# Performance work log

Hardware: AMD Instinct MI355X
Metric: run time of the kernel (lower is better)

The kernel has to match this reference:

```python
import jax, jax.numpy as jnp
import numpy as np

N_HEAD = 16

def setup_inputs() -> dict:
    key = jax.random.key(0)
    k1, k2, k3, k4, k5 = jax.random.split(key, 5)
    B, T, C = 8, 2048, 1024
    hs = C // N_HEAD  # 64
    return {
        "ids": jax.random.normal(k1, (B, T, C), dtype=jnp.float32),
        "qkv_w": jax.random.normal(k2, (3 * hs, C), dtype=jnp.float32) * (C ** -0.5),
        "qkv_b": jax.random.normal(k3, (3 * hs,), dtype=jnp.float32) * 0.02,
        "proj_w": jax.random.normal(k4, (C, C), dtype=jnp.float32) * (C ** -0.5),
        "proj_b": jax.random.normal(k5, (C,), dtype=jnp.float32) * 0.02,
    }

def reference(ids, qkv_w, qkv_b, proj_w, proj_b):
    B, T, C = ids.shape
    hs = qkv_w.shape[0] // 3  # head_size
    # All heads share the same qkv Linear (input is replicated per-head in the
    # original), so compute one head and tile at the end.
    qkv = ids @ qkv_w.T + qkv_b                      # [B,T,3*hs]
    q, k, v = jnp.split(qkv, 3, axis=-1)             # each [B,T,hs]
    wei = jnp.einsum('btd,bsd->bts', q, k)           # [B,T,T]
    tril = jnp.tril(jnp.ones((T, T), dtype=bool))
    wei = jnp.where(tril, wei, jnp.float32(0.0))     # causal mask (no softmax)
    out_h = jnp.einsum('bts,bsd->btd', wei, v)       # [B,T,hs]
    out = jnp.tile(out_h, (1, 1, N_HEAD))            # identical heads concatenated
    return out @ proj_w.T + proj_b                   # [B,T,C]
```

## Files before the change

### kernel.cpp

```cpp
#include <hip/hip_runtime.h>
#include <hip/hip_bf16.h>

#define Bsz 8
#define Tsz 2048
#define Csz 1024
#define HSsz 64
#define NQ 192

typedef __attribute__((ext_vector_type(8))) short short8v;
typedef __attribute__((ext_vector_type(4))) float f32x4;
typedef unsigned short ushortT;
typedef unsigned int uintT;

__device__ __forceinline__ unsigned int f2bf(float f) {
    union { float f; unsigned int u; } v; v.f = f;
    return (v.u + 0x7fffu + ((v.u >> 16) & 1u)) >> 16;
}

__device__ __forceinline__ unsigned int pk2bf(float lo, float hi) {
    union { __hip_bfloat162 h2; unsigned int u; } cv;
    cv.h2 = __float22bfloat162_rn(float2{lo, hi});
    return cv.u;
}

__global__ __launch_bounds__(256) void k_prep(const float* __restrict__ qw,
                                              const float* __restrict__ pw,
                                              ushortT* __restrict__ wB,
                                              ushortT* __restrict__ w2a) {
    const int blk = blockIdx.x;
    if (blk < 96) {
        int idx = blk * 256 + threadIdx.x;
        int l = idx & 63;
        int ksjt = idx >> 6;
        int jt = ksjt % 12, ks = ksjt / 12;
        int j = jt * 16 + (l & 15);
        int k = ks * 32 + (l >> 4) * 8;
        const float* src = &qw[j * Csz + k];
        float4 a = *(const float4*)src;
        float4 b = *(const float4*)(src + 4);
        uint4 o;
        o.x = f2bf(a.x) | (f2bf(a.y) << 16);
        o.y = f2bf(a.z) | (f2bf(a.w) << 16);
        o.z = f2bf(b.x) | (f2bf(b.y) << 16);
        o.w = f2bf(b.z) | (f2bf(b.w) << 16);
        *(uint4*)&wB[(size_t)idx * 8] = o;
    } else {
        int idx = (blk - 96) * 256 + threadIdx.x;
        int l = idx & 63;
        int rest = idx >> 6;
        int m = rest & 63, ks = rest >> 6;
        int c = m * 16 + (l & 15);
        int d0 = ks * 32 + (l >> 4) * 8;
        float s0 = 0, s1 = 0, s2 = 0, s3 = 0, s4 = 0, s5 = 0, s6 = 0, s7 = 0;
#pragma unroll
        for (int hh = 0; hh < 16; ++hh) {
            const float* p = &pw[c * Csz + hh * HSsz + d0];
            float4 x = *(const float4*)p;
            float4 y = *(const float4*)(p + 4);
            s0 += x.x; s1 += x.y; s2 += x.z; s3 += x.w;
            s4 += y.x; s5 += y.y; s6 += y.z; s7 += y.w;
        }
        uint4 o;
        o.x = f2bf(s0) | (f2bf(s1) << 16);
        o.y = f2bf(s2) | (f2bf(s3) << 16);
        o.z = f2bf(s4) | (f2bf(s5) << 16);
        o.w = f2bf(s6) | (f2bf(s7) << 16);
        *(uint4*)&w2a[(size_t)idx * 8] = o;
    }
}

__global__ __launch_bounds__(512, 4) void k_qkv_mfma(const float* __restrict__ ids,
                                                     const ushortT* __restrict__ wB,
                                                     const float* __restrict__ bias,
                                                     ushortT* __restrict__ Qf,
                                                     ushortT* __restrict__ Kf,
                                                     ushortT* __restrict__ Vf) {
    __shared__ float sA[2][32 * 132];
    uintT* Lqk = (uintT*)&sA[0][0];
    uintT* Lv  = Lqk + 32 * 68;

    const int tid = threadIdx.x;
    const int wv  = tid >> 6;
    const int l   = tid & 63;
    const int wm  = wv >> 2;
    const int wn  = wv & 3;
    const int lg  = l >> 4, ll = l & 15;

    const int row0 = blockIdx.x * 32;

    const int srow = tid >> 4;
    const int scol = (tid & 15) * 8;
    const float* gsrc = ids + (size_t)(row0 + srow) * Csz + scol;

    const int afrow = wm * 16 + ll;

    f32x4 acc[3];
    acc[0] = acc[1] = acc[2] = (f32x4){0.f, 0.f, 0.f, 0.f};

    float4 st0 = *(const float4*)gsrc;
    float4 st1 = *(const float4*)(gsrc + 4);

    const ushortT* bbase_p = wB + ((size_t)(wn * 3) * 64 + l) * 8;

    for (int c = 0; c < 8; ++c) {
        float* bufp = &sA[c & 1][0];
        float* wp = &bufp[srow * 132 + scol];
        *(float4*)wp = st0;
        *(float4*)(wp + 4) = st1;
        __syncthreads();
        if (c < 7) {
            st0 = *(const float4*)(gsrc + (c + 1) * 128);
            st1 = *(const float4*)(gsrc + (c + 1) * 128 + 4);
        }
#pragma unroll
        for (int kk = 0; kk < 4; ++kk) {
            const ushortT* bp = bbase_p + (size_t)(4 * c + kk) * 6144;
            short8v b0 = *(const short8v*)(bp);
            short8v b1 = *(const short8v*)(bp + 512);
            short8v b2 = *(const short8v*)(bp + 1024);

            const float* ap = &bufp[afrow * 132 + kk * 32 + lg * 8];
            float4 a0 = *(const float4*)ap;
            float4 a1 = *(const float4*)(ap + 4);
            union { short8v s; unsigned int u[4]; } af;
            af.u[0] = pk2bf(a0.x, a0.y); af.u[1] = pk2bf(a0.z, a0.w);
            af.u[2] = pk2bf(a1.x, a1.y); af.u[3] = pk2bf(a1.z, a1.w);

            acc[0] = __builtin_amdgcn_mfma_f32_16x16x32_bf16(af.s, b0, acc[0], 0, 0, 0);
            acc[1] = __builtin_amdgcn_mfma_f32_16x16x32_bf16(af.s, b1, acc[1], 0, 0, 0);
            acc[2] = __builtin_amdgcn_mfma_f32_16x16x32_bf16(af.s, b2, acc[2], 0, 0, 0);
        }
    }
    __syncthreads();

    const int crow_l = wm * 16 + lg * 4;
    ushortT* L16 = (ushortT*)Lqk;
#pragma unroll
    for (int n = 0; n < 3; ++n) {
        const int jb = wn * 3 + n;
        const int j  = jb * 16 + ll;
        const float bj = bias[j];
        float v0 = acc[n][0] + bj, v1 = acc[n][1] + bj;
        float v2 = acc[n][2] + bj, v3 = acc[n][3] + bj;
        if (jb < 8) {
            ushortT* p = &L16[crow_l * 136 + j];
            p[0]   = (ushortT)f2bf(v0);
            p[136] = (ushortT)f2bf(v1);
            p[272] = (ushortT)f2bf(v2);
            p[408] = (ushortT)f2bf(v3);
        } else {
            uintT* p = &Lv[(j - 128) * 20 + (crow_l >> 1)];
            p[0] = pk2bf(v0, v1);
            p[1] = pk2bf(v2, v3);
        }
    }
    __syncthreads();

    const int l2 = tid & 63, ll2 = l2 & 15, lg2 = l2 >> 4;
    if (tid < 256) {
        const int ks = (tid >> 6) & 1, m = tid >> 7;
        uint4 q = *(const uint4*)&Lqk[(m * 16 + ll2) * 68 + ks * 16 + lg2 * 4];
        *(uint4*)&Qf[(((size_t)(row0 >> 4) + m) * 2 + ks) * 512 + l2 * 8] = q;
        const int n = tid >> 6;
        uint4 v = *(const uint4*)&Lv[(n * 16 + ll2) * 20 + lg2 * 4];
        const int bb = row0 >> 11, s32 = (row0 >> 5) & 63;
        *(uint4*)&Vf[((((size_t)bb * 64 + s32) * 4 + n) * 64 + l2) * 8] = v;
    } else {
        const int ks = (tid >> 6) & 1, m = (tid >> 7) & 1;
        uint4 k = *(const uint4*)&Lqk[(m * 16 + ll2) * 68 + 32 + ks * 16 + lg2 * 4];
        *(uint4*)&Kf[(((size_t)(row0 >> 4) + m) * 2 + ks) * 512 + l2 * 8] = k;
    }
}

__global__ __launch_bounds__(256, 3) void k_attn_mfma(const ushortT* __restrict__ Qf,
                                                      const ushortT* __restrict__ Kf,
                                                      const ushortT* __restrict__ Vf,
                                                      ushortT* __restrict__ hf) {
    __shared__ uintT su[4 * 2 * 16 * 36];
    __shared__ float s_o[4][32 * 68];

    const int tid = threadIdx.x;
    const int w  = tid >> 6;
    const int l  = tid & 63;
    const int lg = l >> 4;
    const int ll = l & 15;

    const int u = blockIdx.x;
    const int b = u / 48;
    const int r = u - b * 48;

    int si, sub, nsub;
    const bool heavy = (r < 32);
    if (heavy) { si = 63 - r; sub = w; nsub = 4; }
    else {
        const int rr = r - 32;
        si = (w < 2) ? (31 - rr) : rr;
        sub = w & 1; nsub = 2;
    }
    const int nT  = (si >> 1) + 1;
    const int qn  = nT / nsub, rem = nT % nsub;
    const int t0  = sub * qn + (sub < rem ? sub : rem);
    const int cnt = qn + (sub < rem ? 1 : 0);

    const int gq = b * 128 + si * 2;

    short8v qf[2][2];
#pragma unroll
    for (int mt = 0; mt < 2; ++mt)
#pragma unroll
        for (int ks = 0; ks < 2; ++ks)
            qf[mt][ks] = *(const short8v*)&Qf[(((size_t)gq + mt) * 2 + ks) * 512 + l * 8];

    f32x4 oacc[2][4];
#pragma unroll
    for (int mt = 0; mt < 2; ++mt)
#pragma unroll
        for (int n = 0; n < 4; ++n) oacc[mt][n] = (f32x4){0.f, 0.f, 0.f, 0.f};

    for (int tile = t0; tile < t0 + cnt; ++tile) {
        const int gs = b * 128 + tile * 4;
        short8v kf[4][2];
#pragma unroll
        for (int ms = 0; ms < 4; ++ms) {
            const ushortT* kp = &Kf[(((size_t)gs + ms) * 2) * 512 + l * 8];
            kf[ms][0] = *(const short8v*)kp;
            kf[ms][1] = *(const short8v*)(kp + 512);
        }
        f32x4 sacc[4][2];
#pragma unroll
        for (int ms = 0; ms < 4; ++ms)
#pragma unroll
            for (int mt = 0; mt < 2; ++mt) sacc[ms][mt] = (f32x4){0.f, 0.f, 0.f, 0.f};
#pragma unroll
        for (int ms = 0; ms < 4; ++ms)
#pragma unroll
            for (int mt = 0; mt < 2; ++mt) {
                sacc[ms][mt] = __builtin_amdgcn_mfma_f32_16x16x32_bf16(kf[ms][0], qf[mt][0], sacc[ms][mt], 0, 0, 0);
                sacc[ms][mt] = __builtin_amdgcn_mfma_f32_16x16x32_bf16(kf[ms][1], qf[mt][1], sacc[ms][mt], 0, 0, 0);
            }
        if (tile == nT - 1) {
#pragma unroll
            for (int ms = 0; ms < 4; ++ms)
#pragma unroll
                for (int mt = 0; mt < 2; ++mt) {
                    const int tg = si * 32 + mt * 16 + ll;
#pragma unroll
                    for (int rr2 = 0; rr2 < 4; ++rr2) {
                        int sg = tile * 64 + ms * 16 + 4 * lg + rr2;
                        if (sg > tg) sacc[ms][mt][rr2] = 0.f;
                    }
                }
        }
#pragma unroll
        for (int mt = 0; mt < 2; ++mt)
#pragma unroll
            for (int ms = 0; ms < 4; ++ms) {
                uint2 pk;
                pk.x = pk2bf(sacc[ms][mt][0], sacc[ms][mt][1]);
                pk.y = pk2bf(sacc[ms][mt][2], sacc[ms][mt][3]);
                *(uint2*)&su[((w * 2 + mt) * 16 + ll) * 36 + ms * 8 + 2 * lg] = pk;
            }
        union { uint4 u4; short8v s; } pa[2][2];
#pragma unroll
        for (int mt = 0; mt < 2; ++mt)
#pragma unroll
            for (int h = 0; h < 2; ++h)
                pa[mt][h].u4 = *(const uint4*)&su[((w * 2 + mt) * 16 + ll) * 36 + h * 16 + lg * 4];

        const int gv = b * 64 + tile * 2;
        short8v vf[2][4];
#pragma unroll
        for (int h = 0; h < 2; ++h)
#pragma unroll
            for (int n = 0; n < 4; ++n)
                vf[h][n] = *(const short8v*)&Vf[((((size_t)gv + h) * 4 + n) * 64 + l) * 8];
#pragma unroll
        for (int mt = 0; mt < 2; ++mt)
#pragma unroll
            for (int n = 0; n < 4; ++n) {
                oacc[mt][n] = __builtin_amdgcn_mfma_f32_16x16x32_bf16(pa[mt][0].s, vf[0][n], oacc[mt][n], 0, 0, 0);
                oacc[mt][n] = __builtin_amdgcn_mfma_f32_16x16x32_bf16(pa[mt][1].s, vf[1][n], oacc[mt][n], 0, 0, 0);
            }
    }

#pragma unroll
    for (int mt = 0; mt < 2; ++mt)
#pragma unroll
        for (int n = 0; n < 4; ++n)
#pragma unroll
            for (int rr2 = 0; rr2 < 4; ++rr2)
                s_o[w][(mt * 16 + 4 * lg + rr2) * 68 + 16 * n + ll] = oacc[mt][n][rr2];
    __syncthreads();

    const int l2 = tid & 63, ll2 = l2 & 15, lg2 = l2 >> 4;
    const int ks = (tid >> 6) & 1, mt = tid >> 7;
    const int t = mt * 16 + ll2, dd = ks * 32 + lg2 * 8;
    if (heavy) {
        float4 A = {0, 0, 0, 0}, B2 = {0, 0, 0, 0};
#pragma unroll
        for (int w2 = 0; w2 < 4; ++w2) {
            const float4 x = *(const float4*)&s_o[w2][t * 68 + dd];
            const float4 y = *(const float4*)&s_o[w2][t * 68 + dd + 4];
            A.x += x.x; A.y += x.y; A.z += x.z; A.w += x.w;
            B2.x += y.x; B2.y += y.y; B2.z += y.z; B2.w += y.w;
        }
        uint4 o;
        o.x = pk2bf(A.x, A.y);  o.y = pk2bf(A.z, A.w);
        o.z = pk2bf(B2.x, B2.y); o.w = pk2bf(B2.z, B2.w);
        *(uint4*)&hf[(((size_t)(b * 128 + si * 2) + mt) * 2 + ks) * 512 + l2 * 8] = o;
    } else {
        const int rr = r - 32;
        const int sa = 31 - rr, sb = rr;
        float4 A = {0, 0, 0, 0}, B2 = {0, 0, 0, 0};
#pragma unroll
        for (int w2 = 0; w2 < 2; ++w2) {
            const float4 x = *(const float4*)&s_o[w2][t * 68 + dd];
            const float4 y = *(const float4*)&s_o[w2][t * 68 + dd + 4];
            A.x += x.x; A.y += x.y; A.z += x.z; A.w += x.w;
            B2.x += y.x; B2.y += y.y; B2.z += y.z; B2.w += y.w;
        }
        uint4 o;
        o.x = pk2bf(A.x, A.y);  o.y = pk2bf(A.z, A.w);
        o.z = pk2bf(B2.x, B2.y); o.w = pk2bf(B2.z, B2.w);
        *(uint4*)&hf[(((size_t)(b * 128 + sa * 2) + mt) * 2 + ks) * 512 + l2 * 8] = o;
        float4 C = {0, 0, 0, 0}, D2 = {0, 0, 0, 0};
#pragma unroll
        for (int w2 = 2; w2 < 4; ++w2) {
            const float4 x = *(const float4*)&s_o[w2][t * 68 + dd];
            const float4 y = *(const float4*)&s_o[w2][t * 68 + dd + 4];
            C.x += x.x; C.y += x.y; C.z += x.z; C.w += x.w;
            D2.x += y.x; D2.y += y.y; D2.z += y.z; D2.w += y.w;
        }
        uint4 o2;
        o2.x = pk2bf(C.x, C.y);  o2.y = pk2bf(C.z, C.w);
        o2.z = pk2bf(D2.x, D2.y); o2.w = pk2bf(D2.z, D2.w);
        *(uint4*)&hf[(((size_t)(b * 128 + sb * 2) + mt) * 2 + ks) * 512 + l2 * 8] = o2;
    }
}

__global__ __launch_bounds__(256) void k_proj_mfma(const ushortT* __restrict__ hf,
                                                   const ushortT* __restrict__ w2a,
                                                   const float* __restrict__ pb,
                                                   float* __restrict__ out) {
    const int tid = threadIdx.x;
    const int w = tid >> 6, l = tid & 63;
    const int t0 = blockIdx.x * 16;
    const size_t M = blockIdx.x;

    short8v hb0 = *(const short8v*)&hf[(M * 2 + 0) * 512 + l * 8];
    short8v hb1 = *(const short8v*)&hf[(M * 2 + 1) * 512 + l * 8];

    const int row = (l >> 4) * 4;
    const int tcol = l & 15;
    const size_t outrow = (size_t)(t0 + tcol) * Csz;

#pragma unroll 2
    for (int m = w * 16; m < w * 16 + 16; ++m) {
        const ushortT* ap = w2a + (size_t)(m * 64 + l) * 8;
        short8v a0 = *(const short8v*)ap;
        short8v a1 = *(const short8v*)(ap + 32768);
        f32x4 acc = (f32x4){0.f, 0.f, 0.f, 0.f};
        acc = __builtin_amdgcn_mfma_f32_16x16x32_bf16(a0, hb0, acc, 0, 0, 0);
        acc = __builtin_amdgcn_mfma_f32_16x16x32_bf16(a1, hb1, acc, 0, 0, 0);
        const int c0 = m * 16 + row;
        const float4 pv = *(const float4*)&pb[c0];
        float4 o;
        o.x = acc[0] + pv.x; o.y = acc[1] + pv.y;
        o.z = acc[2] + pv.z; o.w = acc[3] + pv.w;
        *(float4*)&out[outrow + c0] = o;
    }
}

extern "C" void kernel_launch(void* const* d_in, const int* in_sizes, int n_in,
                              void* d_out, int out_size, void* d_ws, size_t ws_size,
                              hipStream_t stream) {
    const float* ids    = (const float*)d_in[0];
    const float* qkv_w  = (const float*)d_in[1];
    const float* qkv_b  = (const float*)d_in[2];
    const float* proj_w = (const float*)d_in[3];
    const float* proj_b = (const float*)d_in[4];
    float* out = (float*)d_out;

    ushortT* Qf  = (ushortT*)d_ws;
    ushortT* Kf  = Qf + 16384 * HSsz;
    ushortT* Vf  = Kf + 16384 * HSsz;
    ushortT* hf  = Vf + 16384 * HSsz;
    ushortT* wB  = hf + 16384 * HSsz;
    ushortT* w2a = wB + 196608;

    hipLaunchKernelGGL(k_prep,      dim3(128),  dim3(256), 0, stream, qkv_w, proj_w, wB, w2a);
    hipLaunchKernelGGL(k_qkv_mfma,  dim3(512),  dim3(512), 0, stream, ids, wB, qkv_b, Qf, Kf, Vf);
    hipLaunchKernelGGL(k_attn_mfma, dim3(384),  dim3(256), 0, stream, Qf, Kf, Vf, hf);
    hipLaunchKernelGGL(k_proj_mfma, dim3(1024), dim3(256), 0, stream, hf, w2a, proj_b, out);
}
```

Baseline: 63.44 us.

## Simplify attention block scheduling and process two row tiles per projection block

Attention now launches one block per 32-row query tile, ordered heaviest-first, with the four waves splitting key tiles. This replaces the heavy/light pairing scheme and removes its branchy reduction code. The projection kernel handles two 16-row tiles per block so each loaded weight fragment feeds two MFMA chains, halving weight reads and block count. Light attention blocks may leave waves underused, and the projection keeps more accumulators live.

Measured after the change: 60.16 us, median of 2. -5.2%, faster.

```diff
diff --git a/kernel.cpp b/kernel.cpp
--- a/kernel.cpp
+++ b/kernel.cpp
@@ -186,21 +186,13 @@
     const int ll = l & 15;
 
     const int u = blockIdx.x;
-    const int b = u / 48;
-    const int r = u - b * 48;
-
-    int si, sub, nsub;
-    const bool heavy = (r < 32);
-    if (heavy) { si = 63 - r; sub = w; nsub = 4; }
-    else {
-        const int rr = r - 32;
-        si = (w < 2) ? (31 - rr) : rr;
-        sub = w & 1; nsub = 2;
-    }
+    const int b = u & 7;
+    const int si = 63 - (u >> 3);
+
     const int nT  = (si >> 1) + 1;
-    const int qn  = nT / nsub, rem = nT % nsub;
-    const int t0  = sub * qn + (sub < rem ? sub : rem);
-    const int cnt = qn + (sub < rem ? 1 : 0);
+    const int qn  = nT >> 2, rem = nT & 3;
+    const int t0  = w * qn + (w < rem ? w : rem);
+    const int cnt = qn + (w < rem ? 1 : 0);
 
     const int gq = b * 128 + si * 2;
 
@@ -295,47 +287,18 @@
     const int l2 = tid & 63, ll2 = l2 & 15, lg2 = l2 >> 4;
     const int ks = (tid >> 6) & 1, mt = tid >> 7;
     const int t = mt * 16 + ll2, dd = ks * 32 + lg2 * 8;
-    if (heavy) {
-        float4 A = {0, 0, 0, 0}, B2 = {0, 0, 0, 0};
-#pragma unroll
-        for (int w2 = 0; w2 < 4; ++w2) {
-            const float4 x = *(const float4*)&s_o[w2][t * 68 + dd];
-            const float4 y = *(const float4*)&s_o[w2][t * 68 + dd + 4];
-            A.x += x.x; A.y += x.y; A.z += x.z; A.w += x.w;
-            B2.x += y.x; B2.y += y.y; B2.z += y.z; B2.w += y.w;
-        }
-        uint4 o;
-        o.x = pk2bf(A.x, A.y);  o.y = pk2bf(A.z, A.w);
-        o.z = pk2bf(B2.x, B2.y); o.w = pk2bf(B2.z, B2.w);
-        *(uint4*)&hf[(((size_t)(b * 128 + si * 2) + mt) * 2 + ks) * 512 + l2 * 8] = o;
-    } else {
-        const int rr = r - 32;
-        const int sa = 31 - rr, sb = rr;
-        float4 A = {0, 0, 0, 0}, B2 = {0, 0, 0, 0};
-#pragma unroll
-        for (int w2 = 0; w2 < 2; ++w2) {
-            const float4 x = *(const float4*)&s_o[w2][t * 68 + dd];
-            const float4 y = *(const float4*)&s_o[w2][t * 68 + dd + 4];
-            A.x += x.x; A.y += x.y; A.z += x.z; A.w += x.w;
-            B2.x += y.x; B2.y += y.y; B2.z += y.z; B2.w += y.w;
-        }
-        uint4 o;
-        o.x = pk2bf(A.x, A.y);  o.y = pk2bf(A.z, A.w);
-        o.z = pk2bf(B2.x, B2.y); o.w = pk2bf(B2.z, B2.w);
-        *(uint4*)&hf[(((size_t)(b * 128 + sa * 2) + mt) * 2 + ks) * 512 + l2 * 8] = o;
-        float4 C = {0, 0, 0, 0}, D2 = {0, 0, 0, 0};
-#pragma unroll
-        for (int w2 = 2; w2 < 4; ++w2) {
-            const float4 x = *(const float4*)&s_o[w2][t * 68 + dd];
-            const float4 y = *(const float4*)&s_o[w2][t * 68 + dd + 4];
-            C.x += x.x; C.y += x.y; C.z += x.z; C.w += x.w;
-            D2.x += y.x; D2.y += y.y; D2.z += y.z; D2.w += y.w;
-        }
-        uint4 o2;
-        o2.x = pk2bf(C.x, C.y);  o2.y = pk2bf(C.z, C.w);
-        o2.z = pk2bf(D2.x, D2.y); o2.w = pk2bf(D2.z, D2.w);
-        *(uint4*)&hf[(((size_t)(b * 128 + sb * 2) + mt) * 2 + ks) * 512 + l2 * 8] = o2;
-    }
+    float4 A = {0, 0, 0, 0}, B2 = {0, 0, 0, 0};
+#pragma unroll
+    for (int w2 = 0; w2 < 4; ++w2) {
+        const float4 x = *(const float4*)&s_o[w2][t * 68 + dd];
+        const float4 y = *(const float4*)&s_o[w2][t * 68 + dd + 4];
+        A.x += x.x; A.y += x.y; A.z += x.z; A.w += x.w;
+        B2.x += y.x; B2.y += y.y; B2.z += y.z; B2.w += y.w;
+    }
+    uint4 o;
+    o.x = pk2bf(A.x, A.y);  o.y = pk2bf(A.z, A.w);
+    o.z = pk2bf(B2.x, B2.y); o.w = pk2bf(B2.z, B2.w);
+    *(uint4*)&hf[(((size_t)(b * 128 + si * 2) + mt) * 2 + ks) * 512 + l2 * 8] = o;
 }
 
 __global__ __launch_bounds__(256) void k_proj_mfma(const ushortT* __restrict__ hf,
@@ -344,30 +307,40 @@
                                                    float* __restrict__ out) {
     const int tid = threadIdx.x;
     const int w = tid >> 6, l = tid & 63;
-    const int t0 = blockIdx.x * 16;
-    const size_t M = blockIdx.x;
-
-    short8v hb0 = *(const short8v*)&hf[(M * 2 + 0) * 512 + l * 8];
-    short8v hb1 = *(const short8v*)&hf[(M * 2 + 1) * 512 + l * 8];
+    const size_t M0 = (size_t)blockIdx.x * 2;
+
+    short8v hA0 = *(const short8v*)&hf[(M0 * 2 + 0) * 512 + l * 8];
+    short8v hA1 = *(const short8v*)&hf[(M0 * 2 + 1) * 512 + l * 8];
+    short8v hB0 = *(const short8v*)&hf[((M0 + 1) * 2 + 0) * 512 + l * 8];
+    short8v hB1 = *(const short8v*)&hf[((M0 + 1) * 2 + 1) * 512 + l * 8];
 
     const int row = (l >> 4) * 4;
     const int tcol = l & 15;
-    const size_t outrow = (size_t)(t0 + tcol) * Csz;
+    const size_t outA = (M0 * 16 + tcol) * Csz;
+    const size_t outB = ((M0 + 1) * 16 + tcol) * Csz;
 
 #pragma unroll 2
     for (int m = w * 16; m < w * 16 + 16; ++m) {
         const ushortT* ap = w2a + (size_t)(m * 64 + l) * 8;
         short8v a0 = *(const short8v*)ap;
         short8v a1 = *(const short8v*)(ap + 32768);
-        f32x4 acc = (f32x4){0.f, 0.f, 0.f, 0.f};
-        acc = __builtin_amdgcn_mfma_f32_16x16x32_bf16(a0, hb0, acc, 0, 0, 0);
-        acc = __builtin_amdgcn_mfma_f32_16x16x32_bf16(a1, hb1, acc, 0, 0, 0);
         const int c0 = m * 16 + row;
         const float4 pv = *(const float4*)&pb[c0];
-        float4 o;
-        o.x = acc[0] + pv.x; o.y = acc[1] + pv.y;
-        o.z = acc[2] + pv.z; o.w = acc[3] + pv.w;
-        *(float4*)&out[outrow + c0] = o;
+
+        f32x4 accA = (f32x4){0.f, 0.f, 0.f, 0.f};
+        accA = __builtin_amdgcn_mfma_f32_16x16x32_bf16(a0, hA0, accA, 0, 0, 0);
+        accA = __builtin_amdgcn_mfma_f32_16x16x32_bf16(a1, hA1, accA, 0, 0, 0);
+        f32x4 accB = (f32x4){0.f, 0.f, 0.f, 0.f};
+        accB = __builtin_amdgcn_mfma_f32_16x16x32_bf16(a0, hB0, accB, 0, 0, 0);
+        accB = __builtin_amdgcn_mfma_f32_16x16x32_bf16(a1, hB1, accB, 0, 0, 0);
+
+        float4 oA, oB;
+        oA.x = accA[0] + pv.x; oA.y = accA[1] + pv.y;
+        oA.z = accA[2] + pv.z; oA.w = accA[3] + pv.w;
+        oB.x = accB[0] + pv.x; oB.y = accB[1] + pv.y;
+        oB.z = accB[2] + pv.z; oB.w = accB[3] + pv.w;
+        *(float4*)&out[outA + c0] = oA;
+        *(float4*)&out[outB + c0] = oB;
     }
 }
 
@@ -388,8 +361,8 @@
     ushortT* wB  = hf + 16384 * HSsz;
     ushortT* w2a = wB + 196608;
 
-    hipLaunchKernelGGL(k_prep,      dim3(128),  dim3(256), 0, stream, qkv_w, proj_w, wB, w2a);
-    hipLaunchKernelGGL(k_qkv_mfma,  dim3(512),  dim3(512), 0, stream, ids, wB, qkv_b, Qf, Kf, Vf);
-    hipLaunchKernelGGL(k_attn_mfma, dim3(384),  dim3(256), 0, stream, Qf, Kf, Vf, hf);
-    hipLaunchKernelGGL(k_proj_mfma, dim3(1024), dim3(256), 0, stream, hf, w2a, proj_b, out);
-}
+    hipLaunchKernelGGL(k_prep,      dim3(128), dim3(256), 0, stream, qkv_w, proj_w, wB, w2a);
+    hipLaunchKernelGGL(k_qkv_mfma,  dim3(512), dim3(512), 0, stream, ids, wB, qkv_b, Qf, Kf, Vf);
+    hipLaunchKernelGGL(k_attn_mfma, dim3(512), dim3(256), 0, stream, Qf, Kf, Vf, hf);
+    hipLaunchKernelGGL(k_proj_mfma, dim3(512), dim3(256), 0, stream, hf, w2a, proj_b, out);
+}
```
